# Optimization experiments

Hardware: AMD Instinct MI355X
Metric: run time of the kernel (lower is better)

Reference implementation:

```python
import jax, jax.numpy as jnp
import numpy as np

HEADS = 16
HEAD_DIM = 64
DIM = HEADS * HEAD_DIM          # 1024
TEXT_LEN = 226
N_CONCEPTS = 8
FRAMES = 4
PATCHES = 16 * 24               # H*W per latent frame
IMG_LEN = FRAMES * PATCHES      # 1536
TIME_DIM = 512
FF_DIM = 4 * DIM
TOPK_HEADS = 4                  # imap_sep_topk
LN_EPS = 1e-5
QK_EPS = 1e-6


def _layer_norm(x, w, b, eps):
    mu = jnp.mean(x, -1, keepdims=True)
    var = jnp.var(x, -1, keepdims=True)
    return (x - mu) * jax.lax.rsqrt(var + eps) * w + b


def _norm_zero(h, e, temb, lw, lb, nw, nb):
    # CogVideoXLayerNormZero: adaLN shift/scale/gate for hidden and encoder streams
    s = jax.nn.silu(temb) @ lw + lb                      # [B, 6*DIM]
    shift, scale, gate, e_shift, e_scale, e_gate = jnp.split(s, 6, axis=1)
    hn = _layer_norm(h, nw, nb, LN_EPS) * (1 + scale)[:, None] + shift[:, None]
    en = _layer_norm(e, nw, nb, LN_EPS) * (1 + e_scale)[:, None] + e_shift[:, None]
    return hn, en, gate[:, None], e_gate[:, None]


def _heads(x):
    B, S, _ = x.shape
    return x.reshape(B, S, HEADS, HEAD_DIM).transpose(0, 2, 1, 3)


def _rope(x, cos, sin):
    # diffusers apply_rotary_emb, use_real_unbind_dim=-1
    xr = x.reshape(*x.shape[:-1], HEAD_DIM // 2, 2)
    rot = jnp.stack([-xr[..., 1], xr[..., 0]], -1).reshape(x.shape)
    return x * cos + rot * sin


def _sdpa(q, k, v):
    s = jnp.einsum('bhqd,bhkd->bhqk', q, k) * (1.0 / np.sqrt(HEAD_DIM))
    return jnp.einsum('bhqk,bhkd->bhqd', jax.nn.softmax(s, -1), v)


def _attention(norm_h, norm_e, norm_c, rope_cos, rope_sin,
               wq, wk, wv, nq_w, nq_b, nk_w, nk_b, wo, bo):
    B = norm_h.shape[0]
    hs = jnp.concatenate([norm_e, norm_h], axis=1)       # [B, T+P, DIM]
    q, k, v = _heads(hs @ wq), _heads(hs @ wk), _heads(hs @ wv)
    cq, ck, cv = _heads(norm_c @ wq), _heads(norm_c @ wk), _heads(norm_c @ wv)
    q = _layer_norm(q, nq_w, nq_b, QK_EPS); cq = _layer_norm(cq, nq_w, nq_b, QK_EPS)
    k = _layer_norm(k, nk_w, nk_b, QK_EPS); ck = _layer_norm(ck, nk_w, nk_b, QK_EPS)
    q = q.at[:, :, TEXT_LEN:].set(_rope(q[:, :, TEXT_LEN:], rope_cos, rope_sin))
    k = k.at[:, :, TEXT_LEN:].set(_rope(k[:, :, TEXT_LEN:], rope_cos, rope_sin))

    attn_out = _sdpa(q, k, v)                            # [B,H,S,D]
    img_hidden = attn_out[:, :, TEXT_LEN:]               # [B,H,IMG_LEN,D]

    # select_head (reconstructed): per-head spread of image-token activations, top-k heads
    head_score = jnp.std(jnp.mean(img_hidden[1], -1), -1)        # [H]
    _, sel_head_idx = jax.lax.top_k(head_score, TOPK_HEADS)

    iq, ik, iv = q[:, :, TEXT_LEN:], k[:, :, TEXT_LEN:], v[:, :, TEXT_LEN:]
    cat_q = jnp.concatenate([cq, iq], 2)
    cat_k = jnp.concatenate([ck, ik], 2)
    cat_v = jnp.concatenate([cv, iv], 2)
    concept_attn = _sdpa(cat_q, cat_k, cat_v)
    attn_concept = concept_attn[:, :, :N_CONCEPTS]       # [B,H,C,D]

    cross_maps = jnp.mean(jnp.einsum('hpd,hcd->hcp', iq[1], ck[1]), axis=0)
    concept_maps = jnp.sum(jnp.einsum('hcd,hpd->hcp', attn_concept[1], img_hidden[1]), axis=0)

    # select_visual_token (reconstructed): per (head, concept, frame) argmax patch of q.k sim
    text_key = ck[1]                                      # imap_qk_matching_target == 'concept'
    sim = jnp.einsum('hpd,htd->htp', iq[1], text_key).reshape(HEADS, N_CONCEPTS, FRAMES, PATCHES)
    sel_vis_idx = jnp.argmax(sim, axis=-1)                # [H,T,F]

    img_r = img_hidden[1].reshape(HEADS, FRAMES, PATCHES, HEAD_DIM)
    h_ix = jnp.arange(HEADS)[:, None, None]
    f_ix = jnp.arange(FRAMES)[None, None, :]
    sel_img = img_r[h_ix, f_ix, sel_vis_idx]              # [H,T,F,D] gather
    imap = jnp.einsum('htfd,hfpd->htfp', sel_img, img_r)
    imap = (imap - imap.mean(1, keepdims=True)) / (jnp.std(imap, axis=1, keepdims=True, ddof=1) + 1e-6)
    imap = imap.reshape(HEADS, N_CONCEPTS, FRAMES * PATCHES)
    sel_imap = jnp.mean(imap[sel_head_idx], axis=0)       # [T, F*P]
    imap_sum = jnp.sum(imap, axis=0)

    def merge(x):
        return x.transpose(0, 2, 1, 3).reshape(B, x.shape[2], DIM)

    out = merge(attn_out) @ wo + bo
    c_out = merge(attn_concept) @ wo + bo
    return out[:, TEXT_LEN:], out[:, :TEXT_LEN], c_out, sel_imap, imap_sum, concept_maps, cross_maps


def _ff(x, w1, b1, w2, b2):
    return jax.nn.gelu(x @ w1 + b1, approximate=True) @ w2 + b2


def _block(hidden_states, encoder_hidden_states, concept_hidden_states, temb,
           rope_cos, rope_sin,
           norm1_w, norm1_b, ln1_w, ln1_b, norm2_w, norm2_b, ln2_w, ln2_b,
           wq, wk, wv, nq_w, nq_b, nk_w, nk_b, wo, bo,
           ff_w1, ff_b1, ff_w2, ff_b2):
    h, e, c = hidden_states, encoder_hidden_states, concept_hidden_states
    nh, ne, g_msa, eg_msa = _norm_zero(h, e, temb, norm1_w, norm1_b, ln1_w, ln1_b)
    _, nc, _, cg_msa = _norm_zero(h, c, temb, norm1_w, norm1_b, ln1_w, ln1_b)

    a_h, a_e, a_c, sel_imap, imap, concept_maps, cross_maps = _attention(
        nh, ne, nc, rope_cos, rope_sin, wq, wk, wv, nq_w, nq_b, nk_w, nk_b, wo, bo)

    h = h + g_msa * a_h
    e = e + eg_msa * a_e
    c = c + cg_msa * a_c

    nh, ne, g_ff, eg_ff = _norm_zero(h, e, temb, norm2_w, norm2_b, ln2_w, ln2_b)
    _, nc, _, cg_ff = _norm_zero(h, c, temb, norm2_w, norm2_b, ln2_w, ln2_b)

    ff_out = _ff(jnp.concatenate([ne, nh], axis=1), ff_w1, ff_b1, ff_w2, ff_b2)
    ff_c = _ff(nc, ff_w1, ff_b1, ff_w2, ff_b2)
    h = h + g_ff * ff_out[:, TEXT_LEN:]
    e = e + eg_ff * ff_out[:, :TEXT_LEN]
    c = c + cg_ff * ff_c
    return h, e, c, sel_imap, imap, concept_maps, cross_maps


def setup_inputs():
    key = jax.random.key(0)
    ks = jax.random.split(key, 16)
    p = lambda i, shape: jax.random.normal(ks[i], shape, jnp.float32) * 0.02
    return dict(
        hidden_states=jax.random.normal(ks[0], (2, IMG_LEN, DIM), jnp.float32),
        encoder_hidden_states=jax.random.normal(ks[1], (2, TEXT_LEN, DIM), jnp.float32),
        concept_hidden_states=jax.random.normal(ks[2], (2, N_CONCEPTS, DIM), jnp.float32),
        temb=jax.random.normal(ks[3], (2, TIME_DIM), jnp.float32),
        rope_cos=jax.random.uniform(ks[4], (IMG_LEN, HEAD_DIM), jnp.float32),
        rope_sin=jax.random.uniform(ks[5], (IMG_LEN, HEAD_DIM), jnp.float32),
        norm1_w=p(6, (TIME_DIM, 6 * DIM)), norm1_b=jnp.zeros((6 * DIM,), jnp.float32),
        ln1_w=jnp.ones((DIM,), jnp.float32), ln1_b=jnp.zeros((DIM,), jnp.float32),
        norm2_w=p(7, (TIME_DIM, 6 * DIM)), norm2_b=jnp.zeros((6 * DIM,), jnp.float32),
        ln2_w=jnp.ones((DIM,), jnp.float32), ln2_b=jnp.zeros((DIM,), jnp.float32),
        wq=p(8, (DIM, DIM)), wk=p(9, (DIM, DIM)), wv=p(10, (DIM, DIM)),
        nq_w=jnp.ones((HEAD_DIM,), jnp.float32), nq_b=jnp.zeros((HEAD_DIM,), jnp.float32),
        nk_w=jnp.ones((HEAD_DIM,), jnp.float32), nk_b=jnp.zeros((HEAD_DIM,), jnp.float32),
        wo=p(11, (DIM, DIM)), bo=jnp.zeros((DIM,), jnp.float32),
        ff_w1=p(12, (DIM, FF_DIM)), ff_b1=jnp.zeros((FF_DIM,), jnp.float32),
        ff_w2=p(13, (FF_DIM, DIM)), ff_b2=jnp.zeros((DIM,), jnp.float32),
    )


def reference(hidden_states, encoder_hidden_states, concept_hidden_states, temb,
              rope_cos, rope_sin,
              norm1_w, norm1_b, ln1_w, ln1_b, norm2_w, norm2_b, ln2_w, ln2_b,
              wq, wk, wv, nq_w, nq_b, nk_w, nk_b, wo, bo,
              ff_w1, ff_b1, ff_w2, ff_b2):
    return _block(hidden_states, encoder_hidden_states, concept_hidden_states, temb,
                  rope_cos, rope_sin,
                  norm1_w, norm1_b, ln1_w, ln1_b, norm2_w, norm2_b, ln2_w, ln2_b,
                  wq, wk, wv, nq_w, nq_b, nk_w, nk_b, wo, bo,
                  ff_w1, ff_b1, ff_w2, ff_b2)
```

## Files before the change

### kernel.cpp

```cpp
#include <hip/hip_runtime.h>
#include <hip/hip_bf16.h>
#include <math.h>

#define B_ 2
#define HEADS_ 16
#define HD_ 64
#define DIM_ 1024
#define TEXT_ 226
#define NC_ 8
#define FRAMES_ 4
#define PATCHES_ 384
#define IMG_ 1536
#define S_MAIN 1762
#define S2_ 1770
#define TD_ 512
#define FF_ 4096
#define ROWS_ (B_*S2_)
#define VPAD_ 1792

#define OFF_S1   0L
#define OFF_S2   12288L
#define OFF_MISC 24576L
#define OFF_SIM  25600L
#define OFF_IMAP 222208L
#define OFF_AC   418816L
#define OFF_X    435200L
#define OFF_PROJ 4060160L
#define OFF_XN   7685120L
#define OFF_Q    11310080L
#define OFF_K    14935040L
#define OFF_V    18560000L
#define OFF_AO   22184960L
#define OFF_XNB  25809920L

#define O_H    0L
#define O_E    3145728L
#define O_C    3608576L
#define O_SELI 3624960L
#define O_ISUM 3637248L
#define O_CMAP 3649536L
#define O_XMAP 3661824L

typedef __bf16 bf16x8_t __attribute__((ext_vector_type(8)));
typedef float  f32x4_t  __attribute__((ext_vector_type(4)));

__device__ __forceinline__ unsigned int pack2bf(float a, float b) {
    unsigned short ua = __builtin_bit_cast(unsigned short, (__bf16)a);
    unsigned short ub = __builtin_bit_cast(unsigned short, (__bf16)b);
    return (unsigned int)ua | ((unsigned int)ub << 16);
}

__global__ __launch_bounds__(256) void k_silu_mod(
    const float* __restrict__ temb, const float* __restrict__ w1, const float* __restrict__ b1,
    const float* __restrict__ w2, const float* __restrict__ b2,
    float* __restrict__ s1, float* __restrict__ s2)
{
    int gout = blockIdx.x * 64 + (threadIdx.x & 63);
    int ks = threadIdx.x >> 6;
    int which = gout / 12288;
    int r = gout % 12288;
    int b = r / 6144, n = r % 6144;
    const float* w = which ? w2 : w1;
    const float* bb = which ? b2 : b1;
    const float* t = temb + b * TD_;
    float acc = 0.f;
    for (int k = ks*128; k < ks*128 + 128; ++k) {
        float tv = t[k];
        float sv = tv / (1.f + __expf(-tv));
        acc += sv * w[(long)k * 6144 + n];
    }
    __shared__ float red[256];
    red[threadIdx.x] = acc; __syncthreads();
    if (ks == 0) {
        int lt = threadIdx.x;
        float v = red[lt] + red[lt+64] + red[lt+128] + red[lt+192] + bb[n];
        (which ? s2 : s1)[b * 6144 + n] = v;
    }
}

__global__ __launch_bounds__(256) void k_tcvt(
    const float* __restrict__ src, unsigned short* __restrict__ dst, int K, int N)
{
    __shared__ float t[32][33];
    int n0 = blockIdx.x * 32, k0 = blockIdx.y * 32;
    int tx = threadIdx.x & 31, ty = threadIdx.x >> 5;
    #pragma unroll
    for (int i = 0; i < 4; ++i)
        t[ty + 8*i][tx] = src[(size_t)(k0 + ty + 8*i) * N + n0 + tx];
    __syncthreads();
    #pragma unroll
    for (int i = 0; i < 4; ++i) {
        float v = t[tx][ty + 8*i];
        dst[(size_t)(n0 + ty + 8*i) * K + k0 + tx] =
            __builtin_bit_cast(unsigned short, (__bf16)v);
    }
}

__global__ __launch_bounds__(256) void k_tcvt_qkv(
    const float* __restrict__ wq, const float* __restrict__ wk, const float* __restrict__ wv,
    unsigned short* __restrict__ dst)
{
    const float* src = (blockIdx.z == 0) ? wq : (blockIdx.z == 1) ? wk : wv;
    unsigned short* d = dst + (size_t)blockIdx.z * 1024 * 1024;
    __shared__ float t[32][33];
    int n0 = blockIdx.x * 32, k0 = blockIdx.y * 32;
    int tx = threadIdx.x & 31, ty = threadIdx.x >> 5;
    #pragma unroll
    for (int i = 0; i < 4; ++i)
        t[ty + 8*i][tx] = src[(size_t)(k0 + ty + 8*i) * 1024 + n0 + tx];
    __syncthreads();
    #pragma unroll
    for (int i = 0; i < 4; ++i) {
        float v = t[tx][ty + 8*i];
        d[(size_t)(n0 + ty + 8*i) * 1024 + k0 + tx] =
            __builtin_bit_cast(unsigned short, (__bf16)v);
    }
}

__global__ __launch_bounds__(256) void k_vtrans(
    const float* __restrict__ vh, unsigned short* __restrict__ vb)
{
    int bh = blockIdx.z;
    int d0 = blockIdx.y * 32;
    int s0 = blockIdx.x * 32;
    __shared__ float t[32][33];
    int tx = threadIdx.x & 31, ty = threadIdx.x >> 5;
    const float* src = vh + (size_t)bh * S2_ * 64;
    #pragma unroll
    for (int i = 0; i < 4; ++i) {
        int s = s0 + ty + 8*i; if (s >= S2_) s = S2_ - 1;
        t[ty + 8*i][tx] = src[(size_t)s*64 + d0 + tx];
    }
    __syncthreads();
    unsigned short* dst = vb + (size_t)bh * 64 * VPAD_;
    #pragma unroll
    for (int i = 0; i < 4; ++i) {
        int d = d0 + ty + 8*i;
        dst[(size_t)d * VPAD_ + s0 + tx] =
            __builtin_bit_cast(unsigned short, (__bf16)t[tx][ty + 8*i]);
    }
}

__global__ __launch_bounds__(256) void k_ln_mod(
    const float* pe, long bse, const float* ph, long bsh, const float* pc, long bsc,
    const float* __restrict__ smod, const float* __restrict__ lnw, const float* __restrict__ lnb,
    float* __restrict__ out, unsigned short* __restrict__ outb)
{
    long row = blockIdx.x;
    int b = (int)(row / S2_), s = (int)(row % S2_);
    const float* src; int shiftB, scaleB;
    if (s < TEXT_)       { src = pe + (long)b*bse + (long)s*DIM_;          shiftB = 3072; scaleB = 4096; }
    else if (s < S_MAIN) { src = ph + (long)b*bsh + (long)(s-TEXT_)*DIM_;  shiftB = 0;    scaleB = 1024; }
    else                 { src = pc + (long)b*bsc + (long)(s-S_MAIN)*DIM_; shiftB = 3072; scaleB = 4096; }
    int tid = threadIdx.x;
    int col = tid * 4;
    float4 x = *(const float4*)(src + col);
    float lsum = x.x + x.y + x.z + x.w;
    float lsq  = x.x*x.x + x.y*x.y + x.z*x.z + x.w*x.w;
    __shared__ float r1[256], r2[256];
    r1[tid] = lsum; r2[tid] = lsq; __syncthreads();
    for (int st = 128; st; st >>= 1) {
        if (tid < st) { r1[tid] += r1[tid+st]; r2[tid] += r2[tid+st]; }
        __syncthreads();
    }
    float mu = r1[0] * (1.f / DIM_);
    float var = r2[0] * (1.f / DIM_) - mu * mu;
    float rstd = rsqrtf(var + 1e-5f);
    const float* sb = smod + (long)b * 6144;
    float xs[4] = {x.x, x.y, x.z, x.w};
    float res[4];
    #pragma unroll
    for (int i = 0; i < 4; ++i) {
        int cc = col + i;
        float yy = (xs[i] - mu) * rstd * lnw[cc] + lnb[cc];
        res[i] = yy * (1.f + sb[scaleB + cc]) + sb[shiftB + cc];
    }
    if (out)
        *(float4*)(out + row * DIM_ + col) = make_float4(res[0], res[1], res[2], res[3]);
    uint2 pk;
    pk.x = pack2bf(res[0], res[1]); pk.y = pack2bf(res[2], res[3]);
    *(uint2*)(outb + row * DIM_ + col) = pk;
}

__global__ __launch_bounds__(256, 3) void k_bgemm(
    const unsigned short* __restrict__ A, const unsigned short* __restrict__ Wt,
    const float* __restrict__ bias, float* __restrict__ out_f,
    unsigned short* __restrict__ out_b, int M, int N, int K, int kz_len, int mode,
    float* __restrict__ q_out, float* __restrict__ k_out, float* __restrict__ v_out)
{
    __shared__ unsigned short at[2][128*40];
    __shared__ unsigned short bt[2][128*40];
    int tid = threadIdx.x;
    int w = tid >> 6, lane = tid & 63;
    int lr = lane & 15, lh = lane >> 4;
    int wm = w >> 1, wn = w & 1;
    int m0 = blockIdx.y * 128, n0 = blockIdx.x * 128;
    int kbeg = blockIdx.z * kz_len, kend = kbeg + kz_len;

    f32x4_t acc[4][4];
    #pragma unroll
    for (int i = 0; i < 4; ++i)
        #pragma unroll
        for (int j = 0; j < 4; ++j) { acc[i][j][0]=0.f; acc[i][j][1]=0.f; acc[i][j][2]=0.f; acc[i][j][3]=0.f; }

    int srow = tid >> 1, shalf = tid & 1;
    int arow = m0 + srow; if (arow >= M) arow = M - 1;
    const unsigned short* aptr = A + (size_t)arow * K + shalf * 16;
    const unsigned short* bptr = Wt + (size_t)(n0 + srow) * K + shalf * 16;
    int soff = srow * 40 + shalf * 16;

    {
        int4 a0 = *(const int4*)(aptr + kbeg);
        int4 a1 = *(const int4*)(aptr + kbeg + 8);
        int4 b0 = *(const int4*)(bptr + kbeg);
        int4 b1 = *(const int4*)(bptr + kbeg + 8);
        *(int4*)&at[0][soff] = a0; *(int4*)&at[0][soff + 8] = a1;
        *(int4*)&bt[0][soff] = b0; *(int4*)&bt[0][soff + 8] = b1;
    }
    __syncthreads();
    int buf = 0;
    for (int k0 = kbeg; k0 < kend; k0 += 32) {
        bool more = (k0 + 32) < kend;
        int4 na0, na1, nb0, nb1;
        if (more) {
            na0 = *(const int4*)(aptr + k0 + 32);
            na1 = *(const int4*)(aptr + k0 + 40);
            nb0 = *(const int4*)(bptr + k0 + 32);
            nb1 = *(const int4*)(bptr + k0 + 40);
        }
        int4 af[4], bf[4];
        #pragma unroll
        for (int tm = 0; tm < 4; ++tm)
            af[tm] = *(const int4*)&at[buf][(wm*64 + tm*16 + lr)*40 + lh*8];
        #pragma unroll
        for (int tn = 0; tn < 4; ++tn)
            bf[tn] = *(const int4*)&bt[buf][(wn*64 + tn*16 + lr)*40 + lh*8];
        #pragma unroll
        for (int tm = 0; tm < 4; ++tm) {
            bf16x8_t av = __builtin_bit_cast(bf16x8_t, af[tm]);
            #pragma unroll
            for (int tn = 0; tn < 4; ++tn)
                acc[tm][tn] = __builtin_amdgcn_mfma_f32_16x16x32_bf16(
                    av, __builtin_bit_cast(bf16x8_t, bf[tn]), acc[tm][tn], 0, 0, 0);
        }
        if (more) {
            int nb = buf ^ 1;
            *(int4*)&at[nb][soff] = na0; *(int4*)&at[nb][soff + 8] = na1;
            *(int4*)&bt[nb][soff] = nb0; *(int4*)&bt[nb][soff + 8] = nb1;
            __syncthreads();
            buf = nb;
        }
    }
    float* of = out_f;
    if (mode == 1) of += (size_t)blockIdx.z * M * N;
    #pragma unroll
    for (int tm = 0; tm < 4; ++tm) {
        #pragma unroll
        for (int r = 0; r < 4; ++r) {
            int m = m0 + wm*64 + tm*16 + lh*4 + r;
            if (m >= M) continue;
            int b = m / S2_, s = m % S2_;
            #pragma unroll
            for (int tn = 0; tn < 4; ++tn) {
                int n = n0 + wn*64 + tn*16 + lr;
                float v = acc[tm][tn][r];
                if (mode == 0) {
                    int which = n >> 10, c = n & 1023;
                    int hh = c >> 6, d = c & 63;
                    float* dstp = (which == 0) ? q_out : (which == 1) ? k_out : v_out;
                    dstp[(((size_t)b*HEADS_ + hh)*S2_ + s)*64 + d] = v;
                } else if (mode == 1) {
                    of[(size_t)m * N + n] = v + (bias ? bias[n] : 0.f);
                } else {
                    float x = v + bias[n];
                    float u = 0.7978845608028654f * (x + 0.044715f*x*x*x);
                    float g = x / (1.f + __expf(-2.f*u));
                    out_b[(size_t)m * N + n] = __builtin_bit_cast(unsigned short, (__bf16)g);
                }
            }
        }
    }
}

__global__ __launch_bounds__(256) void k_gemm(
    const float* __restrict__ A, const float* __restrict__ W,
    float* __restrict__ C, int M, int N, int K, int kz_len, int headed, int row_off,
    float* __restrict__ part)
{
    __shared__ float As[16][68];
    __shared__ float Bs[16][68];
    int tid = threadIdx.x;
    int bm = blockIdx.y * 64, bn = blockIdx.x * 64;
    int tr = tid >> 4, tc = tid & 15;
    int ar = tid >> 2, akk = (tid & 3) * 4;
    int bkk = tid >> 4, bn4 = (tid & 15) * 4;
    float acc[4][4] = {{0.f}};
    int garow = bm + ar;
    const float* Aptr = A + (size_t)garow * K + akk;
    const float* Wptr = W + (size_t)bkk * N + bn + bn4;
    int kbeg = blockIdx.z * kz_len;
    for (int k0 = kbeg; k0 < kbeg + kz_len; k0 += 16) {
        float4 av = make_float4(0.f, 0.f, 0.f, 0.f);
        if (garow < M) av = *(const float4*)(Aptr + k0);
        As[akk+0][ar] = av.x; As[akk+1][ar] = av.y; As[akk+2][ar] = av.z; As[akk+3][ar] = av.w;
        float4 bv = *(const float4*)(Wptr + (size_t)k0 * N);
        Bs[bkk][bn4+0] = bv.x; Bs[bkk][bn4+1] = bv.y; Bs[bkk][bn4+2] = bv.z; Bs[bkk][bn4+3] = bv.w;
        __syncthreads();
        #pragma unroll
        for (int kk = 0; kk < 16; ++kk) {
            float4 a = *(const float4*)&As[kk][tr*4];
            float4 bq = *(const float4*)&Bs[kk][tc*4];
            float avv[4] = {a.x, a.y, a.z, a.w};
            float bvv[4] = {bq.x, bq.y, bq.z, bq.w};
            #pragma unroll
            for (int i = 0; i < 4; ++i)
                #pragma unroll
                for (int j = 0; j < 4; ++j)
                    acc[i][j] += avv[i] * bvv[j];
        }
        __syncthreads();
    }
    #pragma unroll
    for (int i = 0; i < 4; ++i) {
        int r = bm + tr*4 + i;
        if (r >= M) continue;
        #pragma unroll
        for (int j = 0; j < 4; ++j) {
            int n = bn + tc*4 + j;
            float v = acc[i][j];
            if (part) {
                part[(size_t)blockIdx.z*M*N + (size_t)r*N + n] = v;
            } else if (headed) {
                int rg = r + row_off;
                int b = rg / S2_, s = rg % S2_;
                int hh = n >> 6, d = n & 63;
                C[(((size_t)b*HEADS_ + hh)*S2_ + s)*64 + d] = v;
            } else {
                C[(size_t)(r + row_off) * N + n] = v;
            }
        }
    }
}

__global__ __launch_bounds__(256) void k_fixred(
    const float* __restrict__ pa, float* __restrict__ qh_out)
{
    long i = (long)blockIdx.x*256 + threadIdx.x;
    int r = (int)(i >> 10), n = (int)(i & 1023);
    float v = pa[i] + pa[i + (long)IMG_*DIM_];
    int hh = n >> 6, d = n & 63;
    qh_out[(((size_t)HEADS_ + hh)*S2_ + TEXT_ + r)*64 + d] = v;
}

__global__ __launch_bounds__(256) void k_qk_prep(
    float* qh, float* kh, unsigned short* qbb, unsigned short* kbb,
    const float* __restrict__ nqw, const float* __restrict__ nqb,
    const float* __restrict__ nkw, const float* __restrict__ nkb,
    const float* __restrict__ rc, const float* __restrict__ rs)
{
    int which = blockIdx.y;
    int wid = threadIdx.x >> 6;
    int lane = threadIdx.x & 63;
    long row = (long)blockIdx.x * 4 + wid;
    long s = row % S2_;
    bool b1 = row >= (long)HEADS_*S2_;
    float* base = (which ? kh : qh) + row * 64;
    const float* w  = which ? nkw : nqw;
    const float* bb = which ? nkb : nqb;
    float x = base[lane];
    float sum = x;
    for (int off = 1; off < 64; off <<= 1) sum += __shfl_xor(sum, off, 64);
    float mu = sum * (1.f / 64.f);
    float dx = x - mu;
    float v = dx * dx;
    for (int off = 1; off < 64; off <<= 1) v += __shfl_xor(v, off, 64);
    float rstd = rsqrtf(v * (1.f / 64.f) + 1e-6f);
    float y = dx * rstd * w[lane] + bb[lane];
    if (s >= TEXT_ && s < S_MAIN) {
        long p = s - TEXT_;
        float part = __shfl_xor(y, 1, 64);
        float rot = (lane & 1) ? part : -part;
        y = y * rc[p*64 + lane] + rot * rs[p*64 + lane];
    }
    bool needf = b1 && (which ? (s >= S_MAIN) : (s >= TEXT_ && s < S_MAIN));
    if (needf) base[lane] = y;
    (which ? kbb : qbb)[row * 64 + lane] = __builtin_bit_cast(unsigned short, (__bf16)y);
}

__global__ __launch_bounds__(256) void k_flash(
    const unsigned short* __restrict__ qb, const unsigned short* __restrict__ kb,
    const unsigned short* __restrict__ vb,
    float* __restrict__ ao_out, float* __restrict__ ac_out, int nx_main)
{
    int bx = blockIdx.x;
    int h = blockIdx.y, b = blockIdx.z;
    int qt, NQ, q_off, r0s, r0e, r1s, r1e; float* obase;
    if (bx < nx_main) { qt = bx*128; NQ = S_MAIN; q_off = 0;      r0s = 0;      r0e = S_MAIN; r1s = 0;     r1e = 0;      obase = ao_out; }
    else              { qt = 0;      NQ = NC_;    q_off = S_MAIN; r0s = S_MAIN; r0e = S2_;    r1s = TEXT_; r1e = S_MAIN; obase = ac_out; }
    int tid = threadIdx.x;
    int w = tid >> 6, lane = tid & 63;
    int lr = lane & 15, lh = lane >> 4;
    __shared__ __align__(16) unsigned short kt[64*72];
    __shared__ __align__(16) unsigned short vt[64*72];
    __shared__ __align__(16) unsigned short pbuf[4*32*72];
    unsigned short* pw = pbuf + w*32*72;
    const unsigned short* qbase = qb + (((size_t)b*HEADS_ + h)*S2_ + q_off)*64;
    const unsigned short* kbase = kb + ((size_t)b*HEADS_ + h)*S2_*64;
    const unsigned short* vbase = vb + (size_t)(b*HEADS_ + h)*64*VPAD_;
    bf16x8_t aq[2][2];
    #pragma unroll
    for (int t = 0; t < 2; ++t) {
        int qrow = qt + w*32 + t*16 + lr; if (qrow >= NQ) qrow = NQ - 1;
        const unsigned short* qsrc = qbase + (size_t)qrow*64 + lh*8;
        aq[t][0] = __builtin_bit_cast(bf16x8_t, *(const int4*)qsrc);
        aq[t][1] = __builtin_bit_cast(bf16x8_t, *(const int4*)(qsrc + 32));
    }
    int4 onesi = make_int4(0x3F803F80, 0x3F803F80, 0x3F803F80, 0x3F803F80);
    bf16x8_t bones = __builtin_bit_cast(bf16x8_t, onesi);
    f32x4_t O[2][4];
    f32x4_t Lacc[2];
    #pragma unroll
    for (int t = 0; t < 2; ++t) {
        Lacc[t][0]=0.f; Lacc[t][1]=0.f; Lacc[t][2]=0.f; Lacc[t][3]=0.f;
        #pragma unroll
        for (int g = 0; g < 4; ++g) { O[t][g][0]=0.f; O[t][g][1]=0.f; O[t][g][2]=0.f; O[t][g][3]=0.f; }
    }
    for (int rgi = 0; rgi < 2; ++rgi) {
        int rs = rgi ? r1s : r0s, re = rgi ? r1e : r0e;
        for (int j0 = rs; j0 < re; j0 += 64) {
            int cnt = min(64, re - j0);
            __syncthreads();
            #pragma unroll
            for (int i = 0; i < 2; ++i) {
                int idx = tid + i*256;
                int key = idx >> 3, p8 = idx & 7;
                int krow = j0 + key; if (krow > re - 1) krow = re - 1;
                *(int4*)&kt[key*72 + p8*8] = *(const int4*)(kbase + (size_t)krow*64 + p8*8);
            }
            #pragma unroll
            for (int i = 0; i < 2; ++i) {
                int idx = tid + i*256;
                int d = idx >> 3, p8 = idx & 7;
                *(int4*)&vt[d*72 + p8*8] = *(const int4*)(vbase + (size_t)d*VPAD_ + j0 + p8*8);
            }
            __syncthreads();
            f32x4_t S[2][4];
            #pragma unroll
            for (int g = 0; g < 4; ++g) {
                const unsigned short* kr = &kt[(16*g + lr)*72 + lh*8];
                bf16x8_t b0 = __builtin_bit_cast(bf16x8_t, *(const int4*)kr);
                bf16x8_t b1 = __builtin_bit_cast(bf16x8_t, *(const int4*)(kr + 32));
                #pragma unroll
                for (int t = 0; t < 2; ++t) {
                    f32x4_t z; z[0]=0.f; z[1]=0.f; z[2]=0.f; z[3]=0.f;
                    z = __builtin_amdgcn_mfma_f32_16x16x32_bf16(aq[t][0], b0, z, 0, 0, 0);
                    z = __builtin_amdgcn_mfma_f32_16x16x32_bf16(aq[t][1], b1, z, 0, 0, 0);
                    S[t][g] = z;
                }
            }
            #pragma unroll
            for (int t = 0; t < 2; ++t)
                #pragma unroll
                for (int g = 0; g < 4; ++g) {
                    bool vld = (16*g + lr) < cnt;
                    #pragma unroll
                    for (int r = 0; r < 4; ++r) {
                        float p = vld ? __expf(S[t][g][r] * 0.125f) : 0.f;
                        pw[(t*16 + lh*4 + r)*72 + 16*g + lr] = __builtin_bit_cast(unsigned short, (__bf16)p);
                    }
                }
            #pragma unroll
            for (int c = 0; c < 2; ++c) {
                bf16x8_t ap[2];
                #pragma unroll
                for (int t = 0; t < 2; ++t) {
                    ap[t] = __builtin_bit_cast(bf16x8_t,
                        *(const int4*)&pw[(t*16 + lr)*72 + c*32 + lh*8]);
                    Lacc[t] = __builtin_amdgcn_mfma_f32_16x16x32_bf16(ap[t], bones, Lacc[t], 0, 0, 0);
                }
                #pragma unroll
                for (int g = 0; g < 4; ++g) {
                    bf16x8_t bv = __builtin_bit_cast(bf16x8_t,
                        *(const int4*)&vt[(16*g + lr)*72 + c*32 + lh*8]);
                    #pragma unroll
                    for (int t = 0; t < 2; ++t)
                        O[t][g] = __builtin_amdgcn_mfma_f32_16x16x32_bf16(ap[t], bv, O[t][g], 0, 0, 0);
                }
            }
        }
    }
    #pragma unroll
    for (int t = 0; t < 2; ++t)
        #pragma unroll
        for (int r = 0; r < 4; ++r) {
            float inv = 1.f / Lacc[t][r];
            int gq = qt + w*32 + t*16 + lh*4 + r;
            if (gq < NQ) {
                float* o = obase + (((size_t)b*HEADS_ + h)*NQ + gq)*64 + lr;
                #pragma unroll
                for (int g = 0; g < 4; ++g) o[16*g] = O[t][g][r] * inv;
            }
        }
}

__global__ __launch_bounds__(256) void k_head_score(const float* __restrict__ ao, float* __restrict__ score)
{
    int h = blockIdx.x, tid = threadIdx.x;
    const float* base = ao + (((long)HEADS_ + h)*S_MAIN + TEXT_)*64;
    float sA = 0.f, sB = 0.f;
    for (int p = tid; p < IMG_; p += 256) {
        const float* r = base + (long)p*64;
        float mm = 0.f;
        for (int d = 0; d < 64; d += 4) {
            float4 v = *(const float4*)(r + d);
            mm += v.x + v.y + v.z + v.w;
        }
        mm *= (1.f / 64.f);
        sA += mm; sB += mm*mm;
    }
    __shared__ float r1[256], r2[256];
    r1[tid] = sA; r2[tid] = sB; __syncthreads();
    for (int st = 128; st; st >>= 1) {
        if (tid < st) { r1[tid] += r1[tid+st]; r2[tid] += r2[tid+st]; }
        __syncthreads();
    }
    if (tid == 0) {
        float mean = r1[0] / IMG_, ms = r2[0] / IMG_;
        score[h] = sqrtf(fmaxf(ms - mean*mean, 0.f));
    }
}

__global__ void k_top4(const float* __restrict__ score, int* __restrict__ sel)
{
    if (threadIdx.x == 0 && blockIdx.x == 0) {
        int used = 0;
        for (int k = 0; k < 4; ++k) {
            float best = -INFINITY; int bi = 0;
            for (int h2 = 0; h2 < 16; ++h2) {
                if (used & (1 << h2)) continue;
                if (score[h2] > best) { best = score[h2]; bi = h2; }
            }
            used |= 1 << bi; sel[k] = bi;
        }
    }
}

__global__ __launch_bounds__(512) void k_sim(
    const float* __restrict__ qh, const float* __restrict__ kh,
    float* __restrict__ sim, int* __restrict__ selvis)
{
    int blk = blockIdx.x;
    int h = blk >> 5, t = (blk >> 2) & 7, f = blk & 3;
    int tid = threadIdx.x;
    __shared__ float ckv[64];
    if (tid < 64) ckv[tid] = kh[(((long)HEADS_ + h)*S2_ + S_MAIN + t)*64 + tid];
    __syncthreads();
    float val = -INFINITY; int idx = 0x7fffffff;
    if (tid < PATCHES_) {
        const float* qrow = qh + (((long)HEADS_ + h)*S2_ + TEXT_ + f*PATCHES_ + tid)*64;
        float acc = 0.f;
        for (int d = 0; d < 64; d += 4) {
            float4 qv = *(const float4*)(qrow + d);
            acc += qv.x*ckv[d] + qv.y*ckv[d+1] + qv.z*ckv[d+2] + qv.w*ckv[d+3];
        }
        sim[((long)h*NC_ + t)*IMG_ + f*PATCHES_ + tid] = acc;
        val = acc; idx = tid;
    }
    __shared__ float sv[512]; __shared__ int si[512];
    sv[tid] = val; si[tid] = idx; __syncthreads();
    for (int st = 256; st; st >>= 1) {
        if (tid < st) {
            float v2 = sv[tid+st]; int i2 = si[tid+st];
            if (v2 > sv[tid] || (v2 == sv[tid] && i2 < si[tid])) { sv[tid] = v2; si[tid] = i2; }
        }
        __syncthreads();
    }
    if (tid == 0) selvis[blk] = si[0];
}

__global__ __launch_bounds__(256) void k_cross(const float* __restrict__ sim, float* __restrict__ out)
{
    int i = blockIdx.x*256 + threadIdx.x;
    int c = i / IMG_, p = i % IMG_;
    float acc = 0.f;
    for (int h = 0; h < 16; ++h) acc += sim[((long)h*NC_ + c)*IMG_ + p];
    out[O_XMAP + i] = acc * (1.f / 16.f);
}

__global__ __launch_bounds__(256) void k_concept_maps(
    const float* __restrict__ ac, const float* __restrict__ ao, float* __restrict__ out)
{
    int i = blockIdx.x*256 + threadIdx.x;
    int c = i / IMG_, p = i % IMG_;
    float acc = 0.f;
    for (int h = 0; h < 16; ++h) {
        const float* a = ac + (((long)HEADS_ + h)*NC_ + c)*64;
        const float* g = ao + (((long)HEADS_ + h)*S_MAIN + TEXT_ + p)*64;
        for (int d = 0; d < 64; d += 4) {
            float4 av = *(const float4*)(a + d);
            float4 gv = *(const float4*)(g + d);
            acc += av.x*gv.x + av.y*gv.y + av.z*gv.z + av.w*gv.w;
        }
    }
    out[O_CMAP + i] = acc;
}

__global__ void k_imap_raw(const float* __restrict__ ao, const int* __restrict__ selvis,
                           float* __restrict__ imap)
{
    int blk = blockIdx.x;
    int h = blk >> 5, t = (blk >> 2) & 7, f = blk & 3;
    int tid = threadIdx.x;
    __shared__ float sel[64];
    int pstar = selvis[blk];
    if (tid < 64) sel[tid] = ao[(((long)HEADS_ + h)*S_MAIN + TEXT_ + f*PATCHES_ + pstar)*64 + tid];
    __syncthreads();
    const float* g = ao + (((long)HEADS_ + h)*S_MAIN + TEXT_ + f*PATCHES_ + tid)*64;
    float acc = 0.f;
    for (int d = 0; d < 64; d += 4) {
        float4 gv = *(const float4*)(g + d);
        acc += gv.x*sel[d] + gv.y*sel[d+1] + gv.z*sel[d+2] + gv.w*sel[d+3];
    }
    imap[((long)h*NC_ + t)*IMG_ + f*PATCHES_ + tid] = acc;
}

__global__ __launch_bounds__(256) void k_imap_norm(float* __restrict__ imap)
{
    int i = blockIdx.x*256 + threadIdx.x;
    int h = i / IMG_, fp = i % IMG_;
    float v[8]; float mu = 0.f;
    #pragma unroll
    for (int t = 0; t < 8; ++t) { v[t] = imap[((long)h*NC_ + t)*IMG_ + fp]; mu += v[t]; }
    mu *= 0.125f;
    float var = 0.f;
    #pragma unroll
    for (int t = 0; t < 8; ++t) var += (v[t]-mu)*(v[t]-mu);
    float sd = sqrtf(var * (1.f / 7.f));
    float inv = 1.f / (sd + 1e-6f);
    #pragma unroll
    for (int t = 0; t < 8; ++t) imap[((long)h*NC_ + t)*IMG_ + fp] = (v[t]-mu)*inv;
}

__global__ __launch_bounds__(256) void k_imap_reduce(
    const float* __restrict__ imap, const int* __restrict__ sel, float* __restrict__ out)
{
    int i = blockIdx.x*256 + threadIdx.x;
    int t = i / IMG_, fp = i % IMG_;
    float sum = 0.f;
    for (int h = 0; h < 16; ++h) sum += imap[((long)h*NC_ + t)*IMG_ + fp];
    float ss = 0.f;
    for (int k = 0; k < 4; ++k) { int h = sel[k]; ss += imap[((long)h*NC_ + t)*IMG_ + fp]; }
    out[O_ISUM + i] = sum;
    out[O_SELI + i] = ss * 0.25f;
}

__global__ __launch_bounds__(256) void k_merge(
    const float* __restrict__ ao, const float* __restrict__ ac, unsigned short* __restrict__ xo)
{
    long i = (long)blockIdx.x*256 + threadIdx.x;
    int col = (int)(i & 1023);
    long row = i >> 10;
    int b = (int)(row / S2_), s = (int)(row % S2_);
    int h = col >> 6, d = col & 63;
    float v;
    if (s < S_MAIN) v = ao[(((long)b*HEADS_ + h)*S_MAIN + s)*64 + d];
    else            v = ac[(((long)b*HEADS_ + h)*NC_ + (s - S_MAIN))*64 + d];
    xo[i] = __builtin_bit_cast(unsigned short, (__bf16)v);
}

__global__ __launch_bounds__(256) void k_residual1(
    const float* __restrict__ pe, const float* __restrict__ ph, const float* __restrict__ pc,
    const float* __restrict__ p0, const float* __restrict__ p1, const float* __restrict__ bo,
    const float* __restrict__ s1, float* __restrict__ X)
{
    long i = (long)blockIdx.x*256 + threadIdx.x;
    int col = (int)(i & 1023);
    long row = i >> 10;
    int b = (int)(row / S2_), s = (int)(row % S2_);
    const float* sb = s1 + (long)b * 6144;
    float orig, gate;
    if (s < TEXT_)       { orig = pe[((long)b*TEXT_ + s)*DIM_ + col];            gate = sb[5120 + col]; }
    else if (s < S_MAIN) { orig = ph[((long)b*IMG_ + (s-TEXT_))*DIM_ + col];     gate = sb[2048 + col]; }
    else                 { orig = pc[((long)b*NC_ + (s-S_MAIN))*DIM_ + col];     gate = sb[5120 + col]; }
    X[i] = orig + gate * (p0[i] + p1[i] + bo[col]);
}

__global__ __launch_bounds__(256) void k_final(
    const float* __restrict__ X, const float* __restrict__ f0, const float* __restrict__ f1,
    const float* __restrict__ fb2, const float* __restrict__ s2, float* __restrict__ out)
{
    long i = (long)blockIdx.x*256 + threadIdx.x;
    int col = (int)(i & 1023);
    long row = i >> 10;
    int b = (int)(row / S2_), s = (int)(row % S2_);
    const float* sb = s2 + (long)b * 6144;
    float gate; float* o;
    if (s < TEXT_)       { gate = sb[5120 + col]; o = out + O_E + ((long)b*TEXT_ + s)*DIM_ + col; }
    else if (s < S_MAIN) { gate = sb[2048 + col]; o = out + O_H + ((long)b*IMG_ + (s-TEXT_))*DIM_ + col; }
    else                 { gate = sb[5120 + col]; o = out + O_C + ((long)b*NC_ + (s-S_MAIN))*DIM_ + col; }
    *o = X[i] + gate * (f0[i] + f1[i] + fb2[col]);
}

extern "C" void kernel_launch(void* const* d_in, const int* in_sizes, int n_in,
                              void* d_out, int out_size, void* d_ws, size_t ws_size,
                              hipStream_t stream)
{
    (void)in_sizes; (void)n_in; (void)out_size; (void)ws_size;
    const float* h_in = (const float*)d_in[0];
    const float* e_in = (const float*)d_in[1];
    const float* c_in = (const float*)d_in[2];
    const float* temb = (const float*)d_in[3];
    const float* rcos = (const float*)d_in[4];
    const float* rsin = (const float*)d_in[5];
    const float* n1w  = (const float*)d_in[6];
    const float* n1b  = (const float*)d_in[7];
    const float* ln1w = (const float*)d_in[8];
    const float* ln1b = (const float*)d_in[9];
    const float* n2w  = (const float*)d_in[10];
    const float* n2b  = (const float*)d_in[11];
    const float* ln2w = (const float*)d_in[12];
    const float* ln2b = (const float*)d_in[13];
    const float* wq   = (const float*)d_in[14];
    const float* wk   = (const float*)d_in[15];
    const float* wv   = (const float*)d_in[16];
    const float* nqw  = (const float*)d_in[17];
    const float* nqb  = (const float*)d_in[18];
    const float* nkw  = (const float*)d_in[19];
    const float* nkb  = (const float*)d_in[20];
    const float* wo   = (const float*)d_in[21];
    const float* bo   = (const float*)d_in[22];
    const float* fw1  = (const float*)d_in[23];
    const float* fb1  = (const float*)d_in[24];
    const float* fw2  = (const float*)d_in[25];
    const float* fb2  = (const float*)d_in[26];

    float* ws  = (float*)d_ws;
    float* out = (float*)d_out;
    float* s1   = ws + OFF_S1;
    float* s2   = ws + OFF_S2;
    float* score  = ws + OFF_MISC;
    int*   selh   = (int*)(ws + OFF_MISC + 16);
    int*   selvis = (int*)(ws + OFF_MISC + 32);
    float* sim  = ws + OFF_SIM;
    float* imap = ws + OFF_IMAP;
    float* ac   = ws + OFF_AC;
    float* X    = ws + OFF_X;
    float* proj = ws + OFF_PROJ;
    float* xn   = ws + OFF_XN;
    float* qh   = ws + OFF_Q;
    float* kh   = ws + OFF_K;
    float* vh   = ws + OFF_V;
    float* ao   = ws + OFF_AO;
    float* ffo  = proj;
    float* fixp = ws + OFF_AO;
    unsigned short* xnb   = (unsigned short*)(ws + OFF_XNB);
    unsigned short* wqkvT = (unsigned short*)(ws + OFF_PROJ);
    unsigned short* vb    = (unsigned short*)(ws + OFF_PROJ);
    unsigned short* qbb   = (unsigned short*)(ws + OFF_X);
    unsigned short* kbb   = qbb + (size_t)B_*HEADS_*S2_*64;
    unsigned short* woT   = (unsigned short*)(ws + OFF_AO + 2000000);
    unsigned short* fw1T  = (unsigned short*)(ws + OFF_V);
    unsigned short* fw2T  = (unsigned short*)(ws + OFF_AO);
    unsigned short* ffh   = (unsigned short*)(ws + OFF_Q);

    hipLaunchKernelGGL(k_silu_mod, dim3(384), dim3(256), 0, stream, temb, n1w, n1b, n2w, n2b, s1, s2);
    hipLaunchKernelGGL(k_tcvt_qkv, dim3(32, 32, 3), dim3(256), 0, stream, wq, wk, wv, wqkvT);
    hipLaunchKernelGGL(k_ln_mod, dim3(ROWS_), dim3(256), 0, stream,
        e_in, (long)TEXT_*DIM_, h_in, (long)IMG_*DIM_, c_in, (long)NC_*DIM_, s1, ln1w, ln1b, xn, xnb);
    hipLaunchKernelGGL(k_bgemm, dim3(24, 28, 1), dim3(256), 0, stream,
        xnb, wqkvT, (const float*)nullptr, (float*)nullptr, (unsigned short*)nullptr,
        ROWS_, 3072, 1024, 1024, 0, qh, kh, vh);
    hipLaunchKernelGGL(k_gemm, dim3(16, 24, 2), dim3(256), 0, stream,
        xn + (long)(S2_ + TEXT_)*DIM_, wq, (float*)nullptr, IMG_, DIM_, DIM_, 512, 0, 0, fixp);
    hipLaunchKernelGGL(k_fixred, dim3(6144), dim3(256), 0, stream, fixp, qh);
    hipLaunchKernelGGL(k_gemm, dim3(16, 1, 1), dim3(256), 0, stream,
        xn + (long)(S2_ + S_MAIN)*DIM_, wk, kh, NC_, DIM_, DIM_, 1024, 1, S2_ + S_MAIN, (float*)nullptr);
    hipLaunchKernelGGL(k_qk_prep, dim3(14160, 2), dim3(256), 0, stream,
        qh, kh, qbb, kbb, nqw, nqb, nkw, nkb, rcos, rsin);
    hipLaunchKernelGGL(k_vtrans, dim3(56, 2, 32), dim3(256), 0, stream, vh, vb);
    hipLaunchKernelGGL(k_flash, dim3(15, 16, 2), dim3(256), 0, stream,
        qbb, kbb, vb, ao, ac, 14);
    hipLaunchKernelGGL(k_head_score, dim3(16), dim3(256), 0, stream, ao, score);
    hipLaunchKernelGGL(k_top4, dim3(1), dim3(64), 0, stream, score, selh);
    hipLaunchKernelGGL(k_sim, dim3(512), dim3(512), 0, stream, qh, kh, sim, selvis);
    hipLaunchKernelGGL(k_cross, dim3(48), dim3(256), 0, stream, sim, out);
    hipLaunchKernelGGL(k_concept_maps, dim3(48), dim3(256), 0, stream, ac, ao, out);
    hipLaunchKernelGGL(k_imap_raw, dim3(512), dim3(384), 0, stream, ao, selvis, imap);
    hipLaunchKernelGGL(k_imap_norm, dim3(96), dim3(256), 0, stream, imap);
    hipLaunchKernelGGL(k_imap_reduce, dim3(48), dim3(256), 0, stream, imap, selh, out);
    hipLaunchKernelGGL(k_merge, dim3(14160), dim3(256), 0, stream, ao, ac, xnb);
    hipLaunchKernelGGL(k_tcvt, dim3(32, 32), dim3(256), 0, stream, wo, woT, 1024, 1024);
    hipLaunchKernelGGL(k_bgemm, dim3(8, 28, 2), dim3(256), 0, stream,
        xnb, woT, (const float*)nullptr, proj, (unsigned short*)nullptr, ROWS_, DIM_, 1024, 512, 1,
        (float*)nullptr, (float*)nullptr, (float*)nullptr);
    hipLaunchKernelGGL(k_residual1, dim3(14160), dim3(256), 0, stream,
        e_in, h_in, c_in, proj, proj + (size_t)ROWS_*DIM_, bo, s1, X);
    hipLaunchKernelGGL(k_tcvt, dim3(128, 32), dim3(256), 0, stream, fw1, fw1T, 1024, 4096);
    hipLaunchKernelGGL(k_tcvt, dim3(32, 128), dim3(256), 0, stream, fw2, fw2T, 4096, 1024);
    hipLaunchKernelGGL(k_ln_mod, dim3(ROWS_), dim3(256), 0, stream,
        X, (long)S2_*DIM_, X + (long)TEXT_*DIM_, (long)S2_*DIM_, X + (long)S_MAIN*DIM_, (long)S2_*DIM_,
        s2, ln2w, ln2b, (float*)nullptr, xnb);
    hipLaunchKernelGGL(k_bgemm, dim3(32, 28, 1), dim3(256), 0, stream,
        xnb, fw1T, fb1, (float*)nullptr, ffh, ROWS_, FF_, 1024, 1024, 2,
        (float*)nullptr, (float*)nullptr, (float*)nullptr);
    hipLaunchKernelGGL(k_bgemm, dim3(8, 28, 2), dim3(256), 0, stream,
        ffh, fw2T, (const float*)nullptr, ffo, (unsigned short*)nullptr, ROWS_, DIM_, FF_, 2048, 1,
        (float*)nullptr, (float*)nullptr, (float*)nullptr);
    hipLaunchKernelGGL(k_final, dim3(14160), dim3(256), 0, stream,
        X, ffo, ffo + (size_t)ROWS_*DIM_, fb2, s2, out);
}
```

Baseline: 762.5 us.

## Restructure flash attention into single-wave blocks with register-held K/V and prefetch

The flash kernel now launches one 64-thread wave per 32 query rows instead of 4-wave blocks of 128 rows. K and V tiles move out of shared memory and are loaded straight into registers, and the next K tile is prefetched during the current tile's compute. Block indices are remapped so consecutive blocks are spread across batch-heads, likely for L2/XCD locality. This removes block-wide barriers and LDS staging, but each wave now reloads K/V from global or cache on its own and register pressure goes up.

Result: slower. 781.3 us (+2.5%).

```diff
diff --git a/kernel.cpp b/kernel.cpp
--- a/kernel.cpp
+++ b/kernel.cpp
@@ -387,30 +387,28 @@
     (which ? kbb : qbb)[row * 64 + lane] = __builtin_bit_cast(unsigned short, (__bf16)y);
 }
 
-__global__ __launch_bounds__(256) void k_flash(
+__global__ __launch_bounds__(64) void k_flash(
     const unsigned short* __restrict__ qb, const unsigned short* __restrict__ kb,
     const unsigned short* __restrict__ vb,
-    float* __restrict__ ao_out, float* __restrict__ ac_out, int nx_main)
-{
-    int bx = blockIdx.x;
-    int h = blockIdx.y, b = blockIdx.z;
+    float* __restrict__ ao_out, float* __restrict__ ac_out)
+{
+    int d = blockIdx.x;
+    int bh = (d & 7) * 4 + (d >> 3) / 57;
+    int u  = (d >> 3) % 57;
+    int b = bh >> 4, h = bh & 15;
     int qt, NQ, q_off, r0s, r0e, r1s, r1e; float* obase;
-    if (bx < nx_main) { qt = bx*128; NQ = S_MAIN; q_off = 0;      r0s = 0;      r0e = S_MAIN; r1s = 0;     r1e = 0;      obase = ao_out; }
-    else              { qt = 0;      NQ = NC_;    q_off = S_MAIN; r0s = S_MAIN; r0e = S2_;    r1s = TEXT_; r1e = S_MAIN; obase = ac_out; }
-    int tid = threadIdx.x;
-    int w = tid >> 6, lane = tid & 63;
+    if (u < 56) { qt = u*32; NQ = S_MAIN; q_off = 0;      r0s = 0;      r0e = S_MAIN; r1s = 0;     r1e = 0;      obase = ao_out; }
+    else        { qt = 0;    NQ = NC_;    q_off = S_MAIN; r0s = S_MAIN; r0e = S2_;    r1s = TEXT_; r1e = S_MAIN; obase = ac_out; }
+    int lane = threadIdx.x;
     int lr = lane & 15, lh = lane >> 4;
-    __shared__ __align__(16) unsigned short kt[64*72];
-    __shared__ __align__(16) unsigned short vt[64*72];
-    __shared__ __align__(16) unsigned short pbuf[4*32*72];
-    unsigned short* pw = pbuf + w*32*72;
+    __shared__ __align__(16) unsigned short pw[32*72];
     const unsigned short* qbase = qb + (((size_t)b*HEADS_ + h)*S2_ + q_off)*64;
     const unsigned short* kbase = kb + ((size_t)b*HEADS_ + h)*S2_*64;
     const unsigned short* vbase = vb + (size_t)(b*HEADS_ + h)*64*VPAD_;
     bf16x8_t aq[2][2];
     #pragma unroll
     for (int t = 0; t < 2; ++t) {
-        int qrow = qt + w*32 + t*16 + lr; if (qrow >= NQ) qrow = NQ - 1;
+        int qrow = qt + t*16 + lr; if (qrow >= NQ) qrow = NQ - 1;
         const unsigned short* qsrc = qbase + (size_t)qrow*64 + lh*8;
         aq[t][0] = __builtin_bit_cast(bf16x8_t, *(const int4*)qsrc);
         aq[t][1] = __builtin_bit_cast(bf16x8_t, *(const int4*)(qsrc + 32));
@@ -427,35 +425,48 @@
     }
     for (int rgi = 0; rgi < 2; ++rgi) {
         int rs = rgi ? r1s : r0s, re = rgi ? r1e : r0e;
+        if (rs >= re) continue;
+        int4 kf[8];
+        #pragma unroll
+        for (int g = 0; g < 4; ++g) {
+            int krow = rs + 16*g + lr; if (krow > re - 1) krow = re - 1;
+            const unsigned short* kr = kbase + (size_t)krow*64 + lh*8;
+            kf[2*g]   = *(const int4*)kr;
+            kf[2*g+1] = *(const int4*)(kr + 32);
+        }
         for (int j0 = rs; j0 < re; j0 += 64) {
             int cnt = min(64, re - j0);
-            __syncthreads();
+            int4 vf[8];
             #pragma unroll
-            for (int i = 0; i < 2; ++i) {
-                int idx = tid + i*256;
-                int key = idx >> 3, p8 = idx & 7;
-                int krow = j0 + key; if (krow > re - 1) krow = re - 1;
-                *(int4*)&kt[key*72 + p8*8] = *(const int4*)(kbase + (size_t)krow*64 + p8*8);
-            }
-            #pragma unroll
-            for (int i = 0; i < 2; ++i) {
-                int idx = tid + i*256;
-                int d = idx >> 3, p8 = idx & 7;
-                *(int4*)&vt[d*72 + p8*8] = *(const int4*)(vbase + (size_t)d*VPAD_ + j0 + p8*8);
-            }
-            __syncthreads();
+            for (int c = 0; c < 2; ++c)
+                #pragma unroll
+                for (int g = 0; g < 4; ++g) {
+                    int col = j0 + c*32 + lh*8;
+                    if (col > VPAD_ - 8) col = VPAD_ - 8;
+                    vf[c*4+g] = *(const int4*)(vbase + (size_t)(16*g + lr)*VPAD_ + col);
+                }
             f32x4_t S[2][4];
             #pragma unroll
             for (int g = 0; g < 4; ++g) {
-                const unsigned short* kr = &kt[(16*g + lr)*72 + lh*8];
-                bf16x8_t b0 = __builtin_bit_cast(bf16x8_t, *(const int4*)kr);
-                bf16x8_t b1 = __builtin_bit_cast(bf16x8_t, *(const int4*)(kr + 32));
+                bf16x8_t b0 = __builtin_bit_cast(bf16x8_t, kf[2*g]);
+                bf16x8_t b1 = __builtin_bit_cast(bf16x8_t, kf[2*g+1]);
                 #pragma unroll
                 for (int t = 0; t < 2; ++t) {
                     f32x4_t z; z[0]=0.f; z[1]=0.f; z[2]=0.f; z[3]=0.f;
                     z = __builtin_amdgcn_mfma_f32_16x16x32_bf16(aq[t][0], b0, z, 0, 0, 0);
                     z = __builtin_amdgcn_mfma_f32_16x16x32_bf16(aq[t][1], b1, z, 0, 0, 0);
                     S[t][g] = z;
+                }
+            }
+            bool more = (j0 + 64) < re;
+            int4 kf2[8];
+            if (more) {
+                #pragma unroll
+                for (int g = 0; g < 4; ++g) {
+                    int krow = j0 + 64 + 16*g + lr; if (krow > re - 1) krow = re - 1;
+                    const unsigned short* kr = kbase + (size_t)krow*64 + lh*8;
+                    kf2[2*g]   = *(const int4*)kr;
+                    kf2[2*g+1] = *(const int4*)(kr + 32);
                 }
             }
             #pragma unroll
@@ -480,13 +491,16 @@
                 }
                 #pragma unroll
                 for (int g = 0; g < 4; ++g) {
-                    bf16x8_t bv = __builtin_bit_cast(bf16x8_t,
-                        *(const int4*)&vt[(16*g + lr)*72 + c*32 + lh*8]);
+                    bf16x8_t bv = __builtin_bit_cast(bf16x8_t, vf[c*4+g]);
                     #pragma unroll
                     for (int t = 0; t < 2; ++t)
                         O[t][g] = __builtin_amdgcn_mfma_f32_16x16x32_bf16(ap[t], bv, O[t][g], 0, 0, 0);
                 }
             }
+            if (more) {
+                #pragma unroll
+                for (int i = 0; i < 8; ++i) kf[i] = kf2[i];
+            }
         }
     }
     #pragma unroll
@@ -494,7 +508,7 @@
         #pragma unroll
         for (int r = 0; r < 4; ++r) {
             float inv = 1.f / Lacc[t][r];
-            int gq = qt + w*32 + t*16 + lh*4 + r;
+            int gq = qt + t*16 + lh*4 + r;
             if (gq < NQ) {
                 float* o = obase + (((size_t)b*HEADS_ + h)*NQ + gq)*64 + lr;
                 #pragma unroll
@@ -778,8 +792,8 @@
     hipLaunchKernelGGL(k_qk_prep, dim3(14160, 2), dim3(256), 0, stream,
         qh, kh, qbb, kbb, nqw, nqb, nkw, nkb, rcos, rsin);
     hipLaunchKernelGGL(k_vtrans, dim3(56, 2, 32), dim3(256), 0, stream, vh, vb);
-    hipLaunchKernelGGL(k_flash, dim3(15, 16, 2), dim3(256), 0, stream,
-        qbb, kbb, vb, ao, ac, 14);
+    hipLaunchKernelGGL(k_flash, dim3(1824), dim3(64), 0, stream,
+        qbb, kbb, vb, ao, ac);
     hipLaunchKernelGGL(k_head_score, dim3(16), dim3(256), 0, stream, ao, score);
     hipLaunchKernelGGL(k_top4, dim3(1), dim3(64), 0, stream, score, selh);
     hipLaunchKernelGGL(k_sim, dim3(512), dim3(512), 0, stream, qh, kh, sim, selvis);
```

## Split flash attention key range in two and combine partials in separate kernel

Applied to the files above, without the earlier changes.

Each flash-attention query tile now processes only half of the key range, which doubles the grid from 15 to 30 x-blocks per head and batch. The unnormalised partial outputs and row sums go to scratch buffers reused from vh, xn and sim. A new k_fcomb kernel adds the two partials, divides by the summed denominators and scatters rows into ao and ac. The aim is better CU occupancy during attention, paid for by an extra launch and extra global traffic for the partial buffers.

New measurement: 745.8 us. -2.2%, faster.

```diff
diff --git a/kernel.cpp b/kernel.cpp
--- a/kernel.cpp
+++ b/kernel.cpp
@@ -390,13 +390,23 @@
 __global__ __launch_bounds__(256) void k_flash(
     const unsigned short* __restrict__ qb, const unsigned short* __restrict__ kb,
     const unsigned short* __restrict__ vb,
-    float* __restrict__ ao_out, float* __restrict__ ac_out, int nx_main)
+    float* __restrict__ p0, float* __restrict__ p1, float* __restrict__ pl)
 {
     int bx = blockIdx.x;
     int h = blockIdx.y, b = blockIdx.z;
-    int qt, NQ, q_off, r0s, r0e, r1s, r1e; float* obase;
-    if (bx < nx_main) { qt = bx*128; NQ = S_MAIN; q_off = 0;      r0s = 0;      r0e = S_MAIN; r1s = 0;     r1e = 0;      obase = ao_out; }
-    else              { qt = 0;      NQ = NC_;    q_off = S_MAIN; r0s = S_MAIN; r0e = S2_;    r1s = TEXT_; r1e = S_MAIN; obase = ac_out; }
+    int qt, NQ, q_off, r0s, r0e, r1s, r1e, z;
+    if (bx < 28) {
+        z = bx & 1; int u = bx >> 1;
+        qt = u*128; NQ = S_MAIN; q_off = 0;
+        r0s = z ? 896 : 0; r0e = z ? S_MAIN : 896;
+        r1s = 0; r1e = 0;
+    } else {
+        z = bx - 28;
+        qt = 0; NQ = NC_; q_off = S_MAIN;
+        if (z == 0) { r0s = S_MAIN;      r0e = S2_;    r1s = TEXT_; r1e = TEXT_ + 768; }
+        else        { r0s = TEXT_ + 768; r0e = S_MAIN; r1s = 0;     r1e = 0; }
+    }
+    float* po = z ? p1 : p0;
     int tid = threadIdx.x;
     int w = tid >> 6, lane = tid & 63;
     int lr = lane & 15, lh = lane >> 4;
@@ -452,10 +462,10 @@
                 bf16x8_t b1 = __builtin_bit_cast(bf16x8_t, *(const int4*)(kr + 32));
                 #pragma unroll
                 for (int t = 0; t < 2; ++t) {
-                    f32x4_t z; z[0]=0.f; z[1]=0.f; z[2]=0.f; z[3]=0.f;
-                    z = __builtin_amdgcn_mfma_f32_16x16x32_bf16(aq[t][0], b0, z, 0, 0, 0);
-                    z = __builtin_amdgcn_mfma_f32_16x16x32_bf16(aq[t][1], b1, z, 0, 0, 0);
-                    S[t][g] = z;
+                    f32x4_t zz; zz[0]=0.f; zz[1]=0.f; zz[2]=0.f; zz[3]=0.f;
+                    zz = __builtin_amdgcn_mfma_f32_16x16x32_bf16(aq[t][0], b0, zz, 0, 0, 0);
+                    zz = __builtin_amdgcn_mfma_f32_16x16x32_bf16(aq[t][1], b1, zz, 0, 0, 0);
+                    S[t][g] = zz;
                 }
             }
             #pragma unroll
@@ -493,14 +503,31 @@
     for (int t = 0; t < 2; ++t)
         #pragma unroll
         for (int r = 0; r < 4; ++r) {
-            float inv = 1.f / Lacc[t][r];
             int gq = qt + w*32 + t*16 + lh*4 + r;
             if (gq < NQ) {
-                float* o = obase + (((size_t)b*HEADS_ + h)*NQ + gq)*64 + lr;
+                long rrow = (long)(b*HEADS_ + h)*S2_ + q_off + gq;
+                float* o = po + rrow*64 + lr;
                 #pragma unroll
-                for (int g = 0; g < 4; ++g) o[16*g] = O[t][g][r] * inv;
+                for (int g = 0; g < 4; ++g) o[16*g] = O[t][g][r];
+                if (lr == 0) pl[(long)z*(B_*HEADS_*S2_) + rrow] = Lacc[t][r];
             }
         }
+}
+
+__global__ __launch_bounds__(256) void k_fcomb(
+    const float* __restrict__ p0, const float* __restrict__ p1,
+    const float* __restrict__ pl,
+    float* __restrict__ ao, float* __restrict__ ac)
+{
+    long i = (long)blockIdx.x*256 + threadIdx.x;
+    int d = (int)(i & 63);
+    long rrow = i >> 6;
+    int s = (int)(rrow % S2_);
+    int bh = (int)(rrow / S2_);
+    float l = pl[rrow] + pl[rrow + (long)B_*HEADS_*S2_];
+    float v = (p0[i] + p1[i]) / l;
+    if (s < S_MAIN) ao[((long)bh*S_MAIN + s)*64 + d] = v;
+    else            ac[((long)bh*NC_ + (s - S_MAIN))*64 + d] = v;
 }
 
 __global__ __launch_bounds__(256) void k_head_score(const float* __restrict__ ao, float* __restrict__ score)
@@ -762,6 +789,9 @@
     unsigned short* fw1T  = (unsigned short*)(ws + OFF_V);
     unsigned short* fw2T  = (unsigned short*)(ws + OFF_AO);
     unsigned short* ffh   = (unsigned short*)(ws + OFF_Q);
+    float* fp0 = vh;
+    float* fp1 = xn;
+    float* fpl = sim;
 
     hipLaunchKernelGGL(k_silu_mod, dim3(384), dim3(256), 0, stream, temb, n1w, n1b, n2w, n2b, s1, s2);
     hipLaunchKernelGGL(k_tcvt_qkv, dim3(32, 32, 3), dim3(256), 0, stream, wq, wk, wv, wqkvT);
@@ -778,8 +808,9 @@
     hipLaunchKernelGGL(k_qk_prep, dim3(14160, 2), dim3(256), 0, stream,
         qh, kh, qbb, kbb, nqw, nqb, nkw, nkb, rcos, rsin);
     hipLaunchKernelGGL(k_vtrans, dim3(56, 2, 32), dim3(256), 0, stream, vh, vb);
-    hipLaunchKernelGGL(k_flash, dim3(15, 16, 2), dim3(256), 0, stream,
-        qbb, kbb, vb, ao, ac, 14);
+    hipLaunchKernelGGL(k_flash, dim3(30, 16, 2), dim3(256), 0, stream,
+        qbb, kbb, vb, fp0, fp1, fpl);
+    hipLaunchKernelGGL(k_fcomb, dim3(14160), dim3(256), 0, stream, fp0, fp1, fpl, ao, ac);
     hipLaunchKernelGGL(k_head_score, dim3(16), dim3(256), 0, stream, ao, score);
     hipLaunchKernelGGL(k_top4, dim3(1), dim3(64), 0, stream, score, selh);
     hipLaunchKernelGGL(k_sim, dim3(512), dim3(512), 0, stream, qh, kh, sim, selvis);
```
